# Kernel optimization log

Hardware: AMD Instinct MI355X
Metric: run time of the kernel (lower is better)

Reference implementation:

```python
import jax, jax.numpy as jnp
import numpy as np

N, IN_DIM, HEADS, C = 50000, 78, 10, 78
HC = HEADS * C          # 780
E = 400000
B = 256
NEG_SLOPE = 0.2


def setup_inputs() -> dict:
    key = jax.random.key(0)
    ks = jax.random.split(key, 10)
    x = jax.random.normal(ks[0], (N, IN_DIM), dtype=jnp.float32)
    edge_index = jax.random.randint(ks[1], (2, E), 0, N, dtype=jnp.int64)
    batch = jnp.sort(jax.random.randint(ks[2], (N,), 0, B, dtype=jnp.int64))
    s = 1.0 / np.sqrt(IN_DIM)
    W_l = jax.random.uniform(ks[3], (IN_DIM, HC), jnp.float32, -s, s)
    W_r = jax.random.uniform(ks[4], (IN_DIM, HC), jnp.float32, -s, s)
    att = jax.random.uniform(ks[5], (HEADS, C), jnp.float32, -1.0 / np.sqrt(C), 1.0 / np.sqrt(C))
    bias1 = jnp.zeros((HC,), jnp.float32)
    s2 = 1.0 / np.sqrt(HC)
    W_gcn = jax.random.uniform(ks[6], (HC, HC), jnp.float32, -s2, s2)
    bias_gcn = jnp.zeros((HC,), jnp.float32)
    return {"x": x, "edge_index": edge_index, "batch": batch,
            "W_l": W_l, "W_r": W_r, "att": att, "bias1": bias1,
            "W_gcn": W_gcn, "bias_gcn": bias_gcn}


def _add_self_loops(edge_index, n):
    loops = jnp.arange(n, dtype=edge_index.dtype)
    return jnp.concatenate([edge_index, jnp.stack([loops, loops])], axis=1)


def _gatv2(x, edge_index, W_l, W_r, att, bias):
    ei = _add_self_loops(edge_index, x.shape[0])
    src, dst = ei[0], ei[1]                      # message j -> i
    xl = (x @ W_l).reshape(-1, HEADS, C)         # [N,H,C]
    xr = (x @ W_r).reshape(-1, HEADS, C)
    e = xl[src] + xr[dst]                        # [E',H,C]
    e = jnp.where(e > 0, e, NEG_SLOPE * e)       # leaky_relu
    score = jnp.einsum('ehc,hc->eh', e, att)     # [E',H]
    # segment softmax over destination node
    m = jax.ops.segment_max(score, dst, num_segments=x.shape[0])
    ex = jnp.exp(score - m[dst])
    denom = jax.ops.segment_sum(ex, dst, num_segments=x.shape[0])
    alpha = ex / denom[dst]                      # [E',H]
    out = jax.ops.segment_sum(alpha[:, :, None] * xl[src], dst,
                              num_segments=x.shape[0])  # [N,H,C]
    return out.reshape(-1, HC) + bias


def _gcn(x, edge_index, W, bias):
    n = x.shape[0]
    ei = _add_self_loops(edge_index, n)
    src, dst = ei[0], ei[1]
    deg = jax.ops.segment_sum(jnp.ones_like(src, dtype=x.dtype), dst, num_segments=n)
    dinv = jax.lax.rsqrt(jnp.maximum(deg, 1e-12))
    norm = dinv[src] * dinv[dst]                 # [E']
    h = x @ W
    out = jax.ops.segment_sum(norm[:, None] * h[src], dst, num_segments=n)
    return out + bias


def reference(x, edge_index, batch, W_l, W_r, att, bias1, W_gcn, bias_gcn):
    # eval mode: dropout = identity
    h = jax.nn.elu(_gatv2(x, edge_index, W_l, W_r, att, bias1))
    h = _gcn(h, edge_index, W_gcn, bias_gcn)
    h = jax.nn.relu(h)
    gmax = jax.ops.segment_max(h, batch, num_segments=B)
    gmax = jnp.where(jnp.isfinite(gmax), gmax, 0.0)
    cnt = jax.ops.segment_sum(jnp.ones((h.shape[0], 1), h.dtype), batch, num_segments=B)
    gmean = jax.ops.segment_sum(h, batch, num_segments=B) / jnp.maximum(cnt, 1.0)
    return jnp.concatenate([gmax, gmean], axis=1)   # [B, 2*HC]
```

## Files before the change

### kernel.cpp

```cpp
#include <hip/hip_runtime.h>
#include <hip/hip_bf16.h>
#include <math.h>

#define NNODES   50000
#define INDIM    78
#define NHEADS   10
#define CDIM     78
#define HCDIM    780
#define NEDGES   400000
#define NBATCH   256
#define ETOT     (NEDGES + NNODES)
#define NEG_SLOPE 0.2f

#define BM 128
#define BN 128
#define BK 64
#define KPAD 832
#define NPAD 896
#define LDT 68

#define KP1 128
#define NP1 1664

typedef __attribute__((ext_vector_type(8))) short bf16x8_t;
typedef __attribute__((ext_vector_type(4))) float f32x4_t;
typedef __attribute__((ext_vector_type(2))) float v2f;

__device__ __forceinline__ float bf2f(unsigned short u) {
    union { unsigned int i; float f; } v; v.i = ((unsigned int)u) << 16; return v.f;
}
__device__ __forceinline__ unsigned short f2bf(float f) {
    __hip_bfloat16 h = __float2bfloat16(f);
    return *reinterpret_cast<unsigned short*>(&h);
}
__device__ __forceinline__ v2f cvt2(unsigned int u) {
    union { unsigned int i; float f; } lo, hi;
    lo.i = u << 16;
    hi.i = u & 0xFFFF0000u;
    v2f r; r.x = lo.f; r.y = hi.f; return r;
}
__device__ __forceinline__ v2f vabs2(v2f t) {
    union { v2f f; unsigned long long u; } x; x.f = t;
    x.u &= 0x7FFFFFFF7FFFFFFFull; return x.f;
}
__device__ __forceinline__ float dpp_red16(float x) {
    int y;
    y = __builtin_amdgcn_update_dpp(0, __float_as_int(x), 0xB1, 0xF, 0xF, true);
    x += __int_as_float(y);
    y = __builtin_amdgcn_update_dpp(0, __float_as_int(x), 0x4E, 0xF, 0xF, true);
    x += __int_as_float(y);
    y = __builtin_amdgcn_update_dpp(0, __float_as_int(x), 0x141, 0xF, 0xF, true);
    x += __int_as_float(y);
    y = __builtin_amdgcn_update_dpp(0, __float_as_int(x), 0x140, 0xF, 0xF, true);
    x += __int_as_float(y);
    return x;
}

__device__ __forceinline__ void async_ld16(const unsigned short* g, unsigned short* l) {
    __builtin_amdgcn_global_load_lds(
        (const __attribute__((address_space(1))) void*)g,
        (__attribute__((address_space(3))) void*)l, 16, 0, 0);
}

__global__ void zero_kernel(float* __restrict__ outp, int nf, int* __restrict__ deg, int ni) {
    int i = blockIdx.x * blockDim.x + threadIdx.x;
    if (i < nf) outp[i] = 0.f;
    if (i < ni) deg[i] = 0;
}

__global__ void count_kernel(const int* __restrict__ ei, int* __restrict__ deg) {
    int e = blockIdx.x * blockDim.x + threadIdx.x;
    if (e >= ETOT) return;
    int d = (e < NEDGES) ? ei[NEDGES + e] : (e - NEDGES);
    atomicAdd(&deg[d], 1);
}

__global__ void scan1_kernel(const int* __restrict__ deg, int* __restrict__ rowp,
                             int* __restrict__ bsum) {
    __shared__ int s[256];
    int t = threadIdx.x, b = blockIdx.x;
    int i = b * 256 + t;
    int v = (i < NNODES) ? deg[i] : 0;
    s[t] = v;
    __syncthreads();
    #pragma unroll
    for (int off = 1; off < 256; off <<= 1) {
        int y = (t >= off) ? s[t - off] : 0;
        __syncthreads();
        s[t] += y;
        __syncthreads();
    }
    int incl = s[t];
    if (i < NNODES) rowp[i] = incl - v;
    if (t == 255) bsum[b] = incl;
}

__global__ void scan2_kernel(int* __restrict__ bsum, int* __restrict__ rowp, int nblk,
                             const int* __restrict__ batch, int* __restrict__ bst) {
    __shared__ int s[256];
    int t = threadIdx.x;
    int v = 0;
    if (t < 256) { v = (t < nblk) ? bsum[t] : 0; s[t] = v; }
    __syncthreads();
    #pragma unroll
    for (int off = 1; off < 256; off <<= 1) {
        int y = (t < 256 && t >= off) ? s[t - off] : 0;
        __syncthreads();
        if (t < 256) s[t] += y;
        __syncthreads();
    }
    if (t < 256) {
        int incl = s[t];
        if (t < nblk) bsum[t] = incl - v;
        if (t == 255) rowp[NNODES] = incl;
    } else {
        int b = t - 256;
        int lo = 0, hi = NNODES;
        while (lo < hi) { int mid = (lo + hi) >> 1; if (batch[mid] < b) lo = mid + 1; else hi = mid; }
        bst[b] = lo;
        if (t == 511) bst[NBATCH] = NNODES;
    }
}

__global__ void scan3_kernel(int* __restrict__ rowp, const int* __restrict__ bsum,
                             int* __restrict__ curs, const int* __restrict__ deg,
                             float* __restrict__ dinv) {
    int i = blockIdx.x * 256 + threadIdx.x;
    if (i >= NNODES) return;
    int r = rowp[i] + bsum[i >> 8];
    rowp[i] = r;
    curs[i] = r;
    dinv[i] = rsqrtf((float)deg[i]);
}

__global__ void fill_kernel(const int* __restrict__ ei,
                            int* __restrict__ cursor, int* __restrict__ col) {
    int e = blockIdx.x * blockDim.x + threadIdx.x;
    if (e >= ETOT) return;
    int s, d;
    if (e < NEDGES) { s = ei[e]; d = ei[NEDGES + e]; }
    else            { s = d = e - NEDGES; }
    int pos = atomicAdd(&cursor[d], 1);
    col[pos] = s;
}

__global__ void wprep_kernel(const float* __restrict__ Wl, const float* __restrict__ Wr,
                             unsigned short* __restrict__ Wc) {
    int idx = blockIdx.x * 256 + threadIdx.x;
    if (idx >= NP1 * KP1) return;
    int n = idx >> 7, k = idx & 127;
    float v = 0.f;
    if (k < INDIM) {
        if (n < HCDIM)            v = Wl[(size_t)k * HCDIM + n];
        else if (n < 2 * HCDIM)   v = Wr[(size_t)k * HCDIM + (n - HCDIM)];
    }
    Wc[idx] = f2bf(v);
}

__global__ __launch_bounds__(256) void gemm1_kernel(
        const float* __restrict__ x, const unsigned short* __restrict__ Wc,
        unsigned short* __restrict__ xl, unsigned short* __restrict__ xr, int M) {
    __shared__ unsigned short As[4 * 4096];
    __shared__ unsigned short Bs[4 * 4096];
    int t = threadIdx.x;
    int lane = t & 63, w = t >> 6;
    int bm = blockIdx.x * 128;

    for (int idx = t; idx < 128 * 128; idx += 256) {
        int row = idx >> 7, k = idx & 127;
        int kc = k >> 5, ch = (k >> 3) & 3, e = k & 7;
        int gr = bm + row;
        float v = (gr < M && k < INDIM) ? x[(size_t)gr * INDIM + k] : 0.f;
        As[kc * 4096 + row * 32 + (((ch + (row >> 1)) & 3) * 8) + e] = f2bf(v);
    }

    int lrow = lane >> 2;
    int gch = ((lane & 3) - (lane >> 3)) & 3;
    int m16 = lane & 15, q = lane >> 4;
    int wr = (w >> 1) * 64, wcc = (w & 1) * 64;

    for (int nb = 0; nb < 13; nb++) {
        __syncthreads();
        #pragma unroll
        for (int kc = 0; kc < 4; kc++) {
            const unsigned short* gb = Wc + ((size_t)(nb * 128 + 32 * w + lrow)) * KP1
                                          + kc * 32 + gch * 8;
            unsigned short* lb = Bs + kc * 4096 + (32 * w) * 32;
            async_ld16(gb, lb);
            async_ld16(gb + 16 * KP1, lb + 16 * 32);
        }
        __syncthreads();

        f32x4_t acc[4][4];
        #pragma unroll
        for (int i = 0; i < 4; i++)
            #pragma unroll
            for (int j = 0; j < 4; j++)
                acc[i][j] = (f32x4_t)(0.f);

        #pragma unroll
        for (int kc = 0; kc < 4; kc++) {
            bf16x8_t af[4], bf[4];
            #pragma unroll
            for (int i = 0; i < 4; i++) {
                int row = wr + i * 16 + m16;
                af[i] = *(const bf16x8_t*)&As[kc * 4096 + row * 32 + (((q + (row >> 1)) & 3) * 8)];
            }
            #pragma unroll
            for (int j = 0; j < 4; j++) {
                int row = wcc + j * 16 + m16;
                bf[j] = *(const bf16x8_t*)&Bs[kc * 4096 + row * 32 + (((q + (row >> 1)) & 3) * 8)];
            }
            #pragma unroll
            for (int i = 0; i < 4; i++)
                #pragma unroll
                for (int j = 0; j < 4; j++)
                    acc[i][j] = __builtin_amdgcn_mfma_f32_16x16x32_bf16(af[i], bf[j], acc[i][j], 0, 0, 0);
        }

        #pragma unroll
        for (int j = 0; j < 4; j++) {
            int ng = nb * 128 + wcc + j * 16 + m16;
            if (ng >= 2 * HCDIM) continue;
            unsigned short* dst = (ng < HCDIM) ? (xl + ng) : (xr + (ng - HCDIM));
            #pragma unroll
            for (int i = 0; i < 4; i++) {
                #pragma unroll
                for (int rr = 0; rr < 4; rr++) {
                    int row = bm + wr + i * 16 + q * 4 + rr;
                    if (row < M) dst[(size_t)row * HCDIM] = f2bf(acc[i][j][rr]);
                }
            }
        }
    }
}

__device__ __forceinline__ void gat_body(
        const unsigned int* __restrict__ xp, int cl, bool lo7, bool live,
        v2f r0, v2f r1, v2f r2,
        v2f a60, v2f a61, v2f a62, v2f a40, v2f a41, v2f a42,
        float& l, v2f& acc0, v2f& acc1, v2f& acc2) {
    unsigned int u0 = xp[cl];
    unsigned int u1 = xp[cl + 16];
    unsigned int u2 = lo7 ? xp[cl + 32] : 0u;
    v2f v0 = cvt2(u0), v1 = cvt2(u1), v2v = cvt2(u2);
    v2f t0 = v0 + r0, t1 = v1 + r1, t2 = v2v + r2;
    v2f s2 = t0 * a60 + vabs2(t0) * a40;
    s2 += t1 * a61 + vabs2(t1) * a41;
    s2 += t2 * a62 + vabs2(t2) * a42;
    float part = dpp_red16(s2.x + s2.y);
    float p = __builtin_amdgcn_exp2f(part);
    p = live ? p : 0.f;
    l += p;
    acc0 += p * v0; acc1 += p * v1; acc2 += p * v2v;
}

__global__ __launch_bounds__(256) void gat_kernel(
        const unsigned short* __restrict__ xl, const unsigned short* xr,
        const int* __restrict__ row_ptr, const int* __restrict__ col,
        const float* __restrict__ att, const float* __restrict__ bias1,
        unsigned short* h_out) {
    int wid = blockIdx.x * 4 + (threadIdx.x >> 6);
    int pair = wid / 5;
    int slot = wid - 5 * pair;
    if (pair >= NNODES / 2) return;
    int lane = threadIdx.x & 63;
    int g = lane >> 4, cl = lane & 15;
    bool lo7 = cl < 7;
    bool strad = (slot == 4);
    int node, head;
    if (!strad) { node = 2 * pair + (slot >> 1); head = ((slot & 1) << 2) + g; }
    else        { node = 2 * pair + (g >> 1);    head = 8 + (g & 1); }
    int hcl = head * (CDIM / 2);
    const unsigned int* xlu = (const unsigned int*)xl;
    const unsigned int* xru = (const unsigned int*)xr;

    const float L6 = 0.6f * 1.4426950408889634f;
    const float L4 = 0.4f * 1.4426950408889634f;
    const float2* ap = (const float2*)(att + head * CDIM);
    float2 f0 = ap[cl], f1 = ap[cl + 16];
    float2 f2 = lo7 ? ap[cl + 32] : make_float2(0.f, 0.f);
    v2f a60, a61, a62, a40, a41, a42;
    a60.x = f0.x * L6; a60.y = f0.y * L6;
    a61.x = f1.x * L6; a61.y = f1.y * L6;
    a62.x = f2.x * L6; a62.y = f2.y * L6;
    a40.x = f0.x * L4; a40.y = f0.y * L4;
    a41.x = f1.x * L4; a41.y = f1.y * L4;
    a42.x = f2.x * L4; a42.y = f2.y * L4;

    const unsigned int* xrp = xru + (size_t)node * (HCDIM / 2) + hcl;
    v2f r0 = cvt2(xrp[cl]);
    v2f r1 = cvt2(xrp[cl + 16]);
    v2f r2 = lo7 ? cvt2(xrp[cl + 32]) : (v2f)(0.f);

    float l = 0.f;
    v2f acc0 = (v2f)(0.f), acc1 = (v2f)(0.f), acc2 = (v2f)(0.f);

    if (!strad) {
        int e0 = row_ptr[node], e1 = row_ptr[node + 1];
        int e = e0;
        for (; e + 2 <= e1; e += 2) {
            int ja = __builtin_amdgcn_readfirstlane(col[e]);
            int jb = __builtin_amdgcn_readfirstlane(col[e + 1]);
            gat_body(xlu + (size_t)ja * (HCDIM / 2) + hcl, cl, lo7, true,
                     r0, r1, r2, a60, a61, a62, a40, a41, a42, l, acc0, acc1, acc2);
            gat_body(xlu + (size_t)jb * (HCDIM / 2) + hcl, cl, lo7, true,
                     r0, r1, r2, a60, a61, a62, a40, a41, a42, l, acc0, acc1, acc2);
        }
        if (e < e1) {
            int j = __builtin_amdgcn_readfirstlane(col[e]);
            gat_body(xlu + (size_t)j * (HCDIM / 2) + hcl, cl, lo7, true,
                     r0, r1, r2, a60, a61, a62, a40, a41, a42, l, acc0, acc1, acc2);
        }
    } else {
        int re0 = row_ptr[node], re1 = row_ptr[node + 1];
        int deg = re1 - re0;
        int dA = __builtin_amdgcn_readlane(deg, 0);
        int dB = __builtin_amdgcn_readlane(deg, 32);
        int iters = dA > dB ? dA : dB;
        for (int i = 0; i < iters; i++) {
            bool live = i < deg;
            int ec = re0 + (live ? i : deg - 1);
            int j = col[ec];
            gat_body(xlu + (size_t)j * (HCDIM / 2) + hcl, cl, lo7, live,
                     r0, r1, r2, a60, a61, a62, a40, a41, a42, l, acc0, acc1, acc2);
        }
    }

    float inv = 1.f / l;
    size_t rbase = (size_t)node * HCDIM + head * CDIM;
    const float2* bp = (const float2*)(bias1 + head * CDIM);
    unsigned int* op = (unsigned int*)(h_out + rbase);
    #pragma unroll
    for (int k = 0; k < 3; k++) {
        if (k == 2 && !lo7) break;
        v2f a = (k == 0) ? acc0 : (k == 1) ? acc1 : acc2;
        float2 bb = bp[cl + 16 * k];
        float x0 = a.x * inv + bb.x;
        float x1 = a.y * inv + bb.y;
        x0 = x0 > 0.f ? x0 : (__expf(x0) - 1.f);
        x1 = x1 > 0.f ? x1 : (__expf(x1) - 1.f);
        unsigned int o = (unsigned int)f2bf(x0) | ((unsigned int)f2bf(x1) << 16);
        op[cl + 16 * k] = o;
    }
}

__global__ __launch_bounds__(256) void gcn_agg_kernel(
        const unsigned short* __restrict__ h, const int* __restrict__ row_ptr,
        const int* __restrict__ col, const float* __restrict__ dinv,
        unsigned short* __restrict__ agg) {
    int node = blockIdx.x * 4 + (threadIdx.x >> 6);
    if (node >= NNODES) return;
    int ln = threadIdx.x & 63;
    bool hasC = ln < 3;
    float accA[8] = {}, accB[4] = {}, accC[4] = {};
    int e0 = row_ptr[node], e1 = row_ptr[node + 1];
    int e = e0;
    int jn = (e < e1) ? col[e] : 0;
    for (; e < e1; ) {
        int j = __builtin_amdgcn_readfirstlane(jn);
        ++e;
        jn = (e < e1) ? col[e] : 0;
        float s = dinv[j];
        const unsigned short* hr = h + (size_t)j * HCDIM;
        bf16x8_t u = *(const bf16x8_t*)(hr + 8 * ln);
        ushort4 v4 = *(const ushort4*)(hr + 512 + 4 * ln);
        ushort4 w4 = hasC ? *(const ushort4*)(hr + 768 + 4 * ln) : make_ushort4(0, 0, 0, 0);
        #pragma unroll
        for (int k = 0; k < 8; k++) accA[k] = fmaf(s, bf2f((unsigned short)u[k]), accA[k]);
        accB[0] = fmaf(s, bf2f(v4.x), accB[0]);
        accB[1] = fmaf(s, bf2f(v4.y), accB[1]);
        accB[2] = fmaf(s, bf2f(v4.z), accB[2]);
        accB[3] = fmaf(s, bf2f(v4.w), accB[3]);
        accC[0] = fmaf(s, bf2f(w4.x), accC[0]);
        accC[1] = fmaf(s, bf2f(w4.y), accC[1]);
        accC[2] = fmaf(s, bf2f(w4.z), accC[2]);
        accC[3] = fmaf(s, bf2f(w4.w), accC[3]);
    }
    float di = dinv[node];
    unsigned short* ar = agg + (size_t)node * HCDIM;
    ushort4 o1, o2, ob;
    o1.x = f2bf(accA[0] * di); o1.y = f2bf(accA[1] * di);
    o1.z = f2bf(accA[2] * di); o1.w = f2bf(accA[3] * di);
    o2.x = f2bf(accA[4] * di); o2.y = f2bf(accA[5] * di);
    o2.z = f2bf(accA[6] * di); o2.w = f2bf(accA[7] * di);
    ob.x = f2bf(accB[0] * di); ob.y = f2bf(accB[1] * di);
    ob.z = f2bf(accB[2] * di); ob.w = f2bf(accB[3] * di);
    *(ushort4*)(ar + 8 * ln) = o1;
    *(ushort4*)(ar + 8 * ln + 4) = o2;
    *(ushort4*)(ar + 512 + 4 * ln) = ob;
    if (hasC) {
        ushort4 oc;
        oc.x = f2bf(accC[0] * di); oc.y = f2bf(accC[1] * di);
        oc.z = f2bf(accC[2] * di); oc.w = f2bf(accC[3] * di);
        *(ushort4*)(ar + 768 + 4 * ln) = oc;
    }
}

__global__ void btprep_kernel(const float* __restrict__ W, unsigned short* __restrict__ BT) {
    int idx = blockIdx.x * 256 + threadIdx.x;
    if (idx >= NPAD * KPAD) return;
    int n = idx / KPAD, k = idx - n * KPAD;
    float v = (n < HCDIM && k < HCDIM) ? W[(size_t)k * HCDIM + n] : 0.f;
    BT[idx] = f2bf(v);
}

__global__ __launch_bounds__(256) void gemm2_pool_kernel(
        const unsigned short* __restrict__ A, const unsigned short* __restrict__ BT,
        const float* __restrict__ bias, const int* __restrict__ batch,
        float* __restrict__ out, int M) {
    int f = blockIdx.x;
    int xcd = f & 7, inner = f >> 3;
    int bq = inner / 7, colt = inner - 7 * bq;
    int band = 8 * bq + xcd;
    if (band >= (M + BM - 1) / BM) return;
    int bm = band * BM, bn = colt * BN;

    __shared__ unsigned short smem[2 * 128 * 64];
    unsigned short* As = smem;
    unsigned short* Bs = smem + 128 * 64;
    __shared__ int bsh[BM];

    int t = threadIdx.x;
    int lane = t & 63, w = t >> 6;

    if (t < BM) {
        int row = bm + t;
        bsh[t] = (row < M) ? batch[row] : -1;
    }

    int m16 = lane & 15, q = lane >> 4;
    int wr = (w >> 1) * 64, wc = (w & 1) * 64;

    int lrow8 = lane >> 3;
    int c8 = lane & 7;
    int gch = (c8 - lrow8) & 7;
    const unsigned short* gA = A  + (size_t)(bm + 32 * w + lrow8) * HCDIM + gch * 8;
    const unsigned short* gB = BT + (size_t)(bn + 32 * w + lrow8) * KPAD  + gch * 8;
    unsigned short* lA = As + (32 * w) * 64;
    unsigned short* lB = Bs + (32 * w) * 64;

    f32x4_t acc[4][4];
    #pragma unroll
    for (int i = 0; i < 4; i++)
        #pragma unroll
        for (int j = 0; j < 4; j++)
            acc[i][j] = (f32x4_t)(0.f);

    for (int k0 = 0; k0 < KPAD; k0 += BK) {
        __syncthreads();
        #pragma unroll
        for (int ib = 0; ib < 4; ib++) {
            async_ld16(gA + (size_t)(8 * ib) * HCDIM + k0, lA + (8 * ib) * 64);
            async_ld16(gB + (size_t)(8 * ib) * KPAD  + k0, lB + (8 * ib) * 64);
        }
        __syncthreads();

        #pragma unroll
        for (int half = 0; half < 2; half++) {
            bf16x8_t af[4], bf[4];
            #pragma unroll
            for (int i = 0; i < 4; i++) {
                int row = wr + i * 16 + m16;
                af[i] = *(const bf16x8_t*)&As[row * 64 + ((4 * half + q + row) & 7) * 8];
            }
            #pragma unroll
            for (int j = 0; j < 4; j++) {
                int row = wc + j * 16 + m16;
                bf[j] = *(const bf16x8_t*)&Bs[row * 64 + ((4 * half + q + row) & 7) * 8];
            }
            #pragma unroll
            for (int i = 0; i < 4; i++)
                #pragma unroll
                for (int j = 0; j < 4; j++)
                    acc[i][j] = __builtin_amdgcn_mfma_f32_16x16x32_bf16(af[i], bf[j], acc[i][j], 0, 0, 0);
        }
    }

    float bvj[4];
    #pragma unroll
    for (int j = 0; j < 4; j++) {
        int gcc = bn + wc + j * 16 + m16;
        bvj[j] = (gcc < HCDIM) ? bias[gcc] : 0.f;
    }

    #pragma unroll
    for (int p = 0; p < 2; p++) {
        __syncthreads();
        if ((w >> 1) == p) {
            #pragma unroll
            for (int i = 0; i < 4; i++) {
                #pragma unroll
                for (int j = 0; j < 4; j++) {
                    int colc = wc + j * 16 + m16;
                    ushort4 o;
                    float v0 = acc[i][j][0] + bvj[j];
                    float v1 = acc[i][j][1] + bvj[j];
                    float v2 = acc[i][j][2] + bvj[j];
                    float v3 = acc[i][j][3] + bvj[j];
                    o.x = f2bf(v0 > 0.f ? v0 : 0.f);
                    o.y = f2bf(v1 > 0.f ? v1 : 0.f);
                    o.z = f2bf(v2 > 0.f ? v2 : 0.f);
                    o.w = f2bf(v3 > 0.f ? v3 : 0.f);
                    *(ushort4*)&smem[colc * LDT + i * 16 + q * 4] = o;
                }
            }
        }
        __syncthreads();
        int colp = t & 127;
        int rb = (t >> 7) * 32;
        int gc = bn + colp;
        if (gc < HCDIM) {
            int cur = -1; float mx = 0.f, sm = 0.f;
            bool done = false;
            for (int rr = rb; rr < rb + 32 && !done; rr += 4) {
                ushort4 u = *(const ushort4*)&smem[colp * LDT + rr];
                unsigned short us[4] = {u.x, u.y, u.z, u.w};
                #pragma unroll
                for (int s2 = 0; s2 < 4; s2++) {
                    int b = bsh[64 * p + rr + s2];
                    if (b < 0) { done = true; break; }
                    float v = bf2f(us[s2]);
                    if (b != cur) {
                        if (cur >= 0) {
                            atomicMax((int*)(out + (size_t)cur * (2 * HCDIM) + gc), __float_as_int(mx));
                            atomicAdd(out + (size_t)cur * (2 * HCDIM) + HCDIM + gc, sm);
                        }
                        cur = b; mx = v; sm = v;
                    } else { mx = fmaxf(mx, v); sm += v; }
                }
            }
            if (cur >= 0) {
                atomicMax((int*)(out + (size_t)cur * (2 * HCDIM) + gc), __float_as_int(mx));
                atomicAdd(out + (size_t)cur * (2 * HCDIM) + HCDIM + gc, sm);
            }
        }
    }
}

__global__ void finalize_kernel(float* __restrict__ out, const int* __restrict__ bst) {
    int i = blockIdx.x * blockDim.x + threadIdx.x;
    if (i >= NBATCH * HCDIM) return;
    int b = i / HCDIM, c = i - b * HCDIM;
    int cnt = bst[b + 1] - bst[b];
    out[(size_t)b * (2 * HCDIM) + HCDIM + c] /= (float)(cnt > 0 ? cnt : 1);
}

extern "C" void kernel_launch(void* const* d_in, const int* in_sizes, int n_in,
                              void* d_out, int out_size, void* d_ws, size_t ws_size,
                              hipStream_t stream) {
    const float* x       = (const float*)d_in[0];
    const int*   ei      = (const int*)d_in[1];
    const int*   batch   = (const int*)d_in[2];
    const float* W_l     = (const float*)d_in[3];
    const float* W_r     = (const float*)d_in[4];
    const float* att     = (const float*)d_in[5];
    const float* bias1   = (const float*)d_in[6];
    const float* W_gcn   = (const float*)d_in[7];
    const float* bias_gcn= (const float*)d_in[8];
    float* out = (float*)d_out;

    char* w = (char*)d_ws;
    const size_t BIGH = (size_t)NNODES * HCDIM * sizeof(unsigned short);
    unsigned short* xl  = (unsigned short*)(w);
    unsigned short* xr  = (unsigned short*)(w + BIGH);
    unsigned short* agg = xl;
    unsigned short* BT  = xr;
    char* sm = w + 2 * BIGH;
    int*   rowp = (int*)(sm);                    sm += 50048 * 4;
    int*   col  = (int*)(sm);                    sm += 450048 * 4;
    float* dinv = (float*)(sm);                  sm += 50048 * 4;
    int*   bst  = (int*)(sm);                    sm += 512 * 4;
    int*   bsum = (int*)(sm);                    sm += 256 * 4;
    char* S = sm;                                sm += 426240;
    int*   deg  = (int*)(S);
    int*   curs = (int*)(S + 200192);
    unsigned short* Wc = (unsigned short*)(S);
    size_t needed = (size_t)(sm - (char*)d_ws);
    if (ws_size < needed) return;

    zero_kernel<<<(NBATCH * 2 * HCDIM + 255) / 256, 256, 0, stream>>>(
        out, NBATCH * 2 * HCDIM, deg, NNODES);

    {
        int eblocks = (ETOT + 255) / 256;
        int nblocks = (NNODES + 255) / 256;
        count_kernel<<<eblocks, 256, 0, stream>>>(ei, deg);
        scan1_kernel<<<nblocks, 256, 0, stream>>>(deg, rowp, bsum);
        scan2_kernel<<<1, 512, 0, stream>>>(bsum, rowp, nblocks, batch, bst);
        scan3_kernel<<<nblocks, 256, 0, stream>>>(rowp, bsum, curs, deg, dinv);
        fill_kernel<<<eblocks, 256, 0, stream>>>(ei, curs, col);
    }

    wprep_kernel<<<(NP1 * KP1 + 255) / 256, 256, 0, stream>>>(W_l, W_r, Wc);

    gemm1_kernel<<<(NNODES + 127) / 128, 256, 0, stream>>>(x, Wc, xl, xr, NNODES);

    {
        int waves = (NNODES / 2) * 5;
        int blocks = (waves + 3) / 4;
        gat_kernel<<<blocks, 256, 0, stream>>>(xl, xr, rowp, col, att, bias1, xr);
    }

    gcn_agg_kernel<<<(NNODES + 3) / 4, 256, 0, stream>>>(xr, rowp, col, dinv, agg);

    btprep_kernel<<<(NPAD * KPAD + 255) / 256, 256, 0, stream>>>(W_gcn, BT);

    {
        int nb = (NNODES + BM - 1) / BM;
        int gx = 8 * ((nb + 7) / 8) * 7;
        gemm2_pool_kernel<<<gx, 256, 0, stream>>>(agg, BT, bias_gcn, batch, out, NNODES);
    }

    finalize_kernel<<<(NBATCH * HCDIM + 255) / 256, 256, 0, stream>>>(out, bst);
}
```

Measured before the change: 642.4 us.

## Remap GAT waves to 8 lanes per head and prescale GCN source features

The GAT kernel now gives each head 8 lanes with 5 channel pairs per lane instead of 16 lanes with 3, so one wave covers 8 heads of a single node. Groups of four nodes share a fifth straddle wave for heads 8-9. The reduction becomes 3-step DPP, and the 2-edge unroll is removed. The GAT output is also pre-multiplied by dinv[node], so the GCN aggregation drops the per-edge dinv[j] gather and FMA and uses plain adds. This trades fewer wasted lanes and fewer cross-lane steps for more registers per lane and less edge-level parallelism.

```diff
diff --git a/kernel.cpp b/kernel.cpp
--- a/kernel.cpp
+++ b/kernel.cpp
@@ -43,15 +43,13 @@
     union { v2f f; unsigned long long u; } x; x.f = t;
     x.u &= 0x7FFFFFFF7FFFFFFFull; return x.f;
 }
-__device__ __forceinline__ float dpp_red16(float x) {
+__device__ __forceinline__ float dpp_red8(float x) {
     int y;
     y = __builtin_amdgcn_update_dpp(0, __float_as_int(x), 0xB1, 0xF, 0xF, true);
     x += __int_as_float(y);
     y = __builtin_amdgcn_update_dpp(0, __float_as_int(x), 0x4E, 0xF, 0xF, true);
     x += __int_as_float(y);
     y = __builtin_amdgcn_update_dpp(0, __float_as_int(x), 0x141, 0xF, 0xF, true);
-    x += __int_as_float(y);
-    y = __builtin_amdgcn_update_dpp(0, __float_as_int(x), 0x140, 0xF, 0xF, true);
     x += __int_as_float(y);
     return x;
 }
@@ -235,113 +233,110 @@
     }
 }
 
-__device__ __forceinline__ void gat_body(
-        const unsigned int* __restrict__ xp, int cl, bool lo7, bool live,
-        v2f r0, v2f r1, v2f r2,
-        v2f a60, v2f a61, v2f a62, v2f a40, v2f a41, v2f a42,
-        float& l, v2f& acc0, v2f& acc1, v2f& acc2) {
-    unsigned int u0 = xp[cl];
-    unsigned int u1 = xp[cl + 16];
-    unsigned int u2 = lo7 ? xp[cl + 32] : 0u;
-    v2f v0 = cvt2(u0), v1 = cvt2(u1), v2v = cvt2(u2);
-    v2f t0 = v0 + r0, t1 = v1 + r1, t2 = v2v + r2;
-    v2f s2 = t0 * a60 + vabs2(t0) * a40;
-    s2 += t1 * a61 + vabs2(t1) * a41;
-    s2 += t2 * a62 + vabs2(t2) * a42;
-    float part = dpp_red16(s2.x + s2.y);
-    float p = __builtin_amdgcn_exp2f(part);
-    p = live ? p : 0.f;
-    l += p;
-    acc0 += p * v0; acc1 += p * v1; acc2 += p * v2v;
-}
-
 __global__ __launch_bounds__(256) void gat_kernel(
         const unsigned short* __restrict__ xl, const unsigned short* xr,
         const int* __restrict__ row_ptr, const int* __restrict__ col,
         const float* __restrict__ att, const float* __restrict__ bias1,
-        unsigned short* h_out) {
+        const float* __restrict__ dinv, unsigned short* h_out) {
     int wid = blockIdx.x * 4 + (threadIdx.x >> 6);
-    int pair = wid / 5;
-    int slot = wid - 5 * pair;
-    if (pair >= NNODES / 2) return;
+    int quad = wid / 5;
+    int slot = wid - 5 * quad;
+    if (quad >= NNODES / 4) return;
     int lane = threadIdx.x & 63;
-    int g = lane >> 4, cl = lane & 15;
+    int g = lane >> 3, cl = lane & 7;
     bool lo7 = cl < 7;
     bool strad = (slot == 4);
     int node, head;
-    if (!strad) { node = 2 * pair + (slot >> 1); head = ((slot & 1) << 2) + g; }
-    else        { node = 2 * pair + (g >> 1);    head = 8 + (g & 1); }
+    if (!strad) { node = 4 * quad + slot;      head = g; }
+    else        { node = 4 * quad + (g >> 1);  head = 8 + (g & 1); }
     int hcl = head * (CDIM / 2);
     const unsigned int* xlu = (const unsigned int*)xl;
     const unsigned int* xru = (const unsigned int*)xr;
 
+    int off[5];
+    off[0] = cl; off[1] = cl + 8; off[2] = cl + 16; off[3] = cl + 24;
+    off[4] = lo7 ? cl + 32 : 38;
+
     const float L6 = 0.6f * 1.4426950408889634f;
     const float L4 = 0.4f * 1.4426950408889634f;
     const float2* ap = (const float2*)(att + head * CDIM);
-    float2 f0 = ap[cl], f1 = ap[cl + 16];
-    float2 f2 = lo7 ? ap[cl + 32] : make_float2(0.f, 0.f);
-    v2f a60, a61, a62, a40, a41, a42;
-    a60.x = f0.x * L6; a60.y = f0.y * L6;
-    a61.x = f1.x * L6; a61.y = f1.y * L6;
-    a62.x = f2.x * L6; a62.y = f2.y * L6;
-    a40.x = f0.x * L4; a40.y = f0.y * L4;
-    a41.x = f1.x * L4; a41.y = f1.y * L4;
-    a42.x = f2.x * L4; a42.y = f2.y * L4;
-
     const unsigned int* xrp = xru + (size_t)node * (HCDIM / 2) + hcl;
-    v2f r0 = cvt2(xrp[cl]);
-    v2f r1 = cvt2(xrp[cl + 16]);
-    v2f r2 = lo7 ? cvt2(xrp[cl + 32]) : (v2f)(0.f);
+    v2f a6[5], a4[5], r[5];
+    #pragma unroll
+    for (int k = 0; k < 5; k++) {
+        float2 f = ap[off[k]];
+        if (k == 4 && !lo7) { f.x = 0.f; f.y = 0.f; }
+        a6[k].x = f.x * L6; a6[k].y = f.y * L6;
+        a4[k].x = f.x * L4; a4[k].y = f.y * L4;
+        r[k] = cvt2(xrp[off[k]]);
+    }
 
     float l = 0.f;
-    v2f acc0 = (v2f)(0.f), acc1 = (v2f)(0.f), acc2 = (v2f)(0.f);
+    v2f acc[5];
+    #pragma unroll
+    for (int k = 0; k < 5; k++) acc[k] = (v2f)(0.f);
 
     if (!strad) {
         int e0 = row_ptr[node], e1 = row_ptr[node + 1];
         int e = e0;
-        for (; e + 2 <= e1; e += 2) {
-            int ja = __builtin_amdgcn_readfirstlane(col[e]);
-            int jb = __builtin_amdgcn_readfirstlane(col[e + 1]);
-            gat_body(xlu + (size_t)ja * (HCDIM / 2) + hcl, cl, lo7, true,
-                     r0, r1, r2, a60, a61, a62, a40, a41, a42, l, acc0, acc1, acc2);
-            gat_body(xlu + (size_t)jb * (HCDIM / 2) + hcl, cl, lo7, true,
-                     r0, r1, r2, a60, a61, a62, a40, a41, a42, l, acc0, acc1, acc2);
-        }
-        if (e < e1) {
+        for (; e < e1; e++) {
             int j = __builtin_amdgcn_readfirstlane(col[e]);
-            gat_body(xlu + (size_t)j * (HCDIM / 2) + hcl, cl, lo7, true,
-                     r0, r1, r2, a60, a61, a62, a40, a41, a42, l, acc0, acc1, acc2);
+            const unsigned int* xp = xlu + (size_t)j * (HCDIM / 2) + hcl;
+            v2f v[5], s2 = (v2f)(0.f);
+            #pragma unroll
+            for (int k = 0; k < 5; k++) {
+                v[k] = cvt2(xp[off[k]]);
+                v2f t = v[k] + r[k];
+                s2 += t * a6[k] + vabs2(t) * a4[k];
+            }
+            float p = __builtin_amdgcn_exp2f(dpp_red8(s2.x + s2.y));
+            l += p;
+            #pragma unroll
+            for (int k = 0; k < 5; k++) acc[k] += p * v[k];
         }
     } else {
-        int re0 = row_ptr[node], re1 = row_ptr[node + 1];
-        int deg = re1 - re0;
-        int dA = __builtin_amdgcn_readlane(deg, 0);
-        int dB = __builtin_amdgcn_readlane(deg, 32);
-        int iters = dA > dB ? dA : dB;
+        int re0 = row_ptr[node], deg = row_ptr[node + 1] - re0;
+        int d0 = __builtin_amdgcn_readlane(deg, 0);
+        int d1 = __builtin_amdgcn_readlane(deg, 16);
+        int d2 = __builtin_amdgcn_readlane(deg, 32);
+        int d3 = __builtin_amdgcn_readlane(deg, 48);
+        int iters = max(max(d0, d1), max(d2, d3));
         for (int i = 0; i < iters; i++) {
             bool live = i < deg;
-            int ec = re0 + (live ? i : deg - 1);
+            int ec = re0 + (live ? i : 0);
             int j = col[ec];
-            gat_body(xlu + (size_t)j * (HCDIM / 2) + hcl, cl, lo7, live,
-                     r0, r1, r2, a60, a61, a62, a40, a41, a42, l, acc0, acc1, acc2);
+            const unsigned int* xp = xlu + (size_t)j * (HCDIM / 2) + hcl;
+            v2f v[5], s2 = (v2f)(0.f);
+            #pragma unroll
+            for (int k = 0; k < 5; k++) {
+                v[k] = cvt2(xp[off[k]]);
+                v2f t = v[k] + r[k];
+                s2 += t * a6[k] + vabs2(t) * a4[k];
+            }
+            float p = __builtin_amdgcn_exp2f(dpp_red8(s2.x + s2.y));
+            p = live ? p : 0.f;
+            l += p;
+            #pragma unroll
+            for (int k = 0; k < 5; k++) acc[k] += p * v[k];
         }
     }
 
     float inv = 1.f / l;
+    float dn = dinv[node];
     size_t rbase = (size_t)node * HCDIM + head * CDIM;
     const float2* bp = (const float2*)(bias1 + head * CDIM);
     unsigned int* op = (unsigned int*)(h_out + rbase);
     #pragma unroll
-    for (int k = 0; k < 3; k++) {
-        if (k == 2 && !lo7) break;
-        v2f a = (k == 0) ? acc0 : (k == 1) ? acc1 : acc2;
-        float2 bb = bp[cl + 16 * k];
-        float x0 = a.x * inv + bb.x;
-        float x1 = a.y * inv + bb.y;
+    for (int k = 0; k < 5; k++) {
+        if (k == 4 && !lo7) break;
+        float2 bb = bp[off[k]];
+        float x0 = acc[k].x * inv + bb.x;
+        float x1 = acc[k].y * inv + bb.y;
         x0 = x0 > 0.f ? x0 : (__expf(x0) - 1.f);
         x1 = x1 > 0.f ? x1 : (__expf(x1) - 1.f);
+        x0 *= dn; x1 *= dn;
         unsigned int o = (unsigned int)f2bf(x0) | ((unsigned int)f2bf(x1) << 16);
-        op[cl + 16 * k] = o;
+        op[off[k]] = o;
     }
 }
 
@@ -361,21 +356,20 @@
         int j = __builtin_amdgcn_readfirstlane(jn);
         ++e;
         jn = (e < e1) ? col[e] : 0;
-        float s = dinv[j];
         const unsigned short* hr = h + (size_t)j * HCDIM;
         bf16x8_t u = *(const bf16x8_t*)(hr + 8 * ln);
         ushort4 v4 = *(const ushort4*)(hr + 512 + 4 * ln);
         ushort4 w4 = hasC ? *(const ushort4*)(hr + 768 + 4 * ln) : make_ushort4(0, 0, 0, 0);
         #pragma unroll
-        for (int k = 0; k < 8; k++) accA[k] = fmaf(s, bf2f((unsigned short)u[k]), accA[k]);
-        accB[0] = fmaf(s, bf2f(v4.x), accB[0]);
-        accB[1] = fmaf(s, bf2f(v4.y), accB[1]);
-        accB[2] = fmaf(s, bf2f(v4.z), accB[2]);
-        accB[3] = fmaf(s, bf2f(v4.w), accB[3]);
-        accC[0] = fmaf(s, bf2f(w4.x), accC[0]);
-        accC[1] = fmaf(s, bf2f(w4.y), accC[1]);
-        accC[2] = fmaf(s, bf2f(w4.z), accC[2]);
-        accC[3] = fmaf(s, bf2f(w4.w), accC[3]);
+        for (int k = 0; k < 8; k++) accA[k] += bf2f((unsigned short)u[k]);
+        accB[0] += bf2f(v4.x);
+        accB[1] += bf2f(v4.y);
+        accB[2] += bf2f(v4.z);
+        accB[3] += bf2f(v4.w);
+        accC[0] += bf2f(w4.x);
+        accC[1] += bf2f(w4.y);
+        accC[2] += bf2f(w4.z);
+        accC[3] += bf2f(w4.w);
     }
     float di = dinv[node];
     unsigned short* ar = agg + (size_t)node * HCDIM;
@@ -597,9 +591,9 @@
     gemm1_kernel<<<(NNODES + 127) / 128, 256, 0, stream>>>(x, Wc, xl, xr, NNODES);
 
     {
-        int waves = (NNODES / 2) * 5;
-        int blocks = (waves + 3) / 4;
-        gat_kernel<<<blocks, 256, 0, stream>>>(xl, xr, rowp, col, att, bias1, xr);
+        int waves = (NNODES / 4) * 5;
+        int blocks = waves / 4;
+        gat_kernel<<<blocks, 256, 0, stream>>>(xl, xr, rowp, col, att, bias1, dinv, xr);
     }
 
     gcn_agg_kernel<<<(NNODES + 3) / 4, 256, 0, stream>>>(xr, rowp, col, dinv, agg);
```

Result: no change. 647.5 us (+0.8%).
